# Kernel tuning notes

Hardware: AMD Instinct MI355X
Metric: run time of the kernel (lower is better)

The kernel has to match this reference:

```python
import jax, jax.numpy as jnp
import numpy as np

B, N, D = 4, 2048, 512

def setup_inputs() -> dict:
    key = jax.random.key(0)
    ks = jax.random.split(key, 7)
    s = 1.0 / np.sqrt(D)
    return {
        "x": jax.random.normal(ks[0], (B, N, D), dtype=jnp.float32),
        "Wq": jax.random.uniform(ks[1], (D, D), jnp.float32, -s, s),
        "bq": jax.random.uniform(ks[2], (D,), jnp.float32, -s, s),
        "Wk": jax.random.uniform(ks[3], (D, D), jnp.float32, -s, s),
        "bk": jax.random.uniform(ks[4], (D,), jnp.float32, -s, s),
        "Wv": jax.random.uniform(ks[5], (D, D), jnp.float32, -s, s),
        "bv": jax.random.uniform(ks[6], (D,), jnp.float32, -s, s),
    }

def reference(x, Wq, bq, Wk, bk, Wv, bv):
    # QKV projections (torch Linear: y = x @ W^T + b)
    q = jnp.einsum('bnd,ed->bne', x, Wq) + bq
    k = jnp.einsum('bnd,ed->bne', x, Wk) + bk
    v = jnp.einsum('bnd,ed->bne', x, Wv) + bv
    scale = 1.0 / jnp.sqrt(jnp.asarray(q.shape[-1], q.dtype))
    scores = jnp.einsum('bqd,bkd->bqk', q, k) * scale  # [B,N,N]
    weights = jax.nn.softmax(scores, axis=-1)
    return jnp.einsum('bqk,bkd->bqd', weights, v)
```

## Files before the change

### kernel.cpp

```cpp
#include <hip/hip_runtime.h>
#include <cstdint>
#include <cstddef>

#define SEQ 2048
#define DIM 512

using floatx4 = __attribute__((ext_vector_type(4))) float;
using halfx8  = __attribute__((ext_vector_type(8))) _Float16;

__device__ __forceinline__ ushort f2h(float f) {
    _Float16 h = (_Float16)f;
    return __builtin_bit_cast(unsigned short, h);
}

#define GLL(g, l) __builtin_amdgcn_global_load_lds( \
    (const __attribute__((address_space(1))) uint32_t*)(g), \
    (__attribute__((address_space(3))) uint32_t*)(l), 16, 0, 0)

__global__ void prep_k(const float* __restrict__ x,
                       const float* __restrict__ Wq, const float* __restrict__ Wk,
                       const float* __restrict__ Wv,
                       const float* __restrict__ bq, const float* __restrict__ bk,
                       const float* __restrict__ bv,
                       ushort* __restrict__ xh, ushort* __restrict__ wcat,
                       float* __restrict__ bcat, float* __restrict__ rowsum) {
    int i = blockIdx.x * 256 + threadIdx.x;
    if (i < 1048576) {
        float4 v = ((const float4*)x)[i];
        ((ushort4*)xh)[i] = make_ushort4(f2h(v.x), f2h(v.y), f2h(v.z), f2h(v.w));
    } else if (i < 1048576 + 196608) {
        int j = i - 1048576;
        int which = j >> 16;
        const float* w = (which == 0) ? Wq : (which == 1) ? Wk : Wv;
        float4 v = ((const float4*)w)[j & 0xFFFF];
        ((ushort4*)wcat)[j] = make_ushort4(f2h(v.x), f2h(v.y), f2h(v.z), f2h(v.w));
    } else if (i < 1048576 + 196608 + 384) {
        int j = i - 1245184;
        const float* bsrc = (j < 128) ? bq : (j < 256) ? bk : bv;
        ((float4*)bcat)[j] = ((const float4*)bsrc)[j & 127];
    } else if (i < 1048576 + 196608 + 384 + 2048) {
        int j = i - 1245568;
        ((float4*)rowsum)[j] = (float4){0.f, 0.f, 0.f, 0.f};
    }
}


template<int EPI, int TM>
__global__ __launch_bounds__(TM * 2, 4)
void gemm_k(const ushort* __restrict__ A, const ushort* __restrict__ B,
            void* __restrict__ Cout, const float* __restrict__ bias,
            float* __restrict__ rowsum, ushort* __restrict__ vt,
            int lda, int ldb, int ldc, int kIters, float alpha,
            long sA, long sB, long sC)
{
    constexpr int T = TM * 2;
    __shared__ __align__(16) ushort smem[TM * 64 + 128 * 64];
    ushort* Ps = smem;

    const int tid = threadIdx.x;
    const int bz = blockIdx.z;
    int b, kofs;
    if (EPI == 2) { b = bz & 3; kofs = (bz >> 2) * 1024; }
    else          { b = bz; kofs = 0; }
    const ushort* Ab = A + (size_t)b * sA + kofs;
    const ushort* Bb = B + (size_t)b * sB + kofs;

    const int m0 = blockIdx.y * TM;
    const int n0 = blockIdx.x * 128;
    const int lane = tid & 63, wave = tid >> 6;
    const int wm = (wave >> 1) * 64, wn = (wave & 1) * 64;
    const int quad = lane >> 4, l16 = lane & 15;
    const int swz = (l16 >> 1) & 3;

    const int sA0 = tid, sA1 = tid + T;
    const int rA0 = sA0 >> 2, rA1 = sA1 >> 2;
    const int kA0 = (sA0 & 3) ^ ((rA0 >> 1) & 3);
    const int kA1 = (sA1 & 3) ^ ((rA1 >> 1) & 3);
    const ushort* gA0 = Ab + (size_t)(m0 + rA0) * lda + kA0 * 8;
    const ushort* gA1 = Ab + (size_t)(m0 + rA1) * lda + kA1 * 8;
    const int rB0 = tid >> 2;
    const int kB0 = (tid & 3) ^ ((rB0 >> 1) & 3);
    const ushort* gB0 = Bb + (size_t)(n0 + rB0) * ldb + kB0 * 8;
    const ushort* gB1 = nullptr;
    int sB1 = 0;
    if constexpr (TM == 128) {
        sB1 = tid + 256;
        int rB1 = sB1 >> 2;
        int kB1 = (sB1 & 3) ^ ((rB1 >> 1) & 3);
        gB1 = Bb + (size_t)(n0 + rB1) * ldb + kB1 * 8;
    }

    auto STAGE = [&](int kk, int bufi) {
        int ko = kk * 32;
        ushort* Ad = smem + bufi * (TM * 32);
        ushort* Bd = smem + TM * 64 + bufi * 4096;
        GLL(gA0 + ko, Ad + sA0 * 8);
        GLL(gA1 + ko, Ad + sA1 * 8);
        GLL(gB0 + ko, Bd + tid * 8);
        if constexpr (TM == 128) GLL(gB1 + ko, Bd + sB1 * 8);
    };

    int ofsA[4], ofsB[4];
#pragma unroll
    for (int mi = 0; mi < 4; mi++)
        ofsA[mi] = ((wm + mi * 16 + l16) * 4 + (quad ^ swz)) * 8;
#pragma unroll
    for (int ni = 0; ni < 4; ni++)
        ofsB[ni] = ((wn + ni * 16 + l16) * 4 + (quad ^ swz)) * 8;

    floatx4 acc[4][4];
#pragma unroll
    for (int i = 0; i < 4; i++)
#pragma unroll
        for (int j = 0; j < 4; j++)
            acc[i][j] = (floatx4){0.f, 0.f, 0.f, 0.f};

    STAGE(0, 0);
    for (int it = 0; it < kIters; ++it) {
        __syncthreads();
        const int buf = it & 1;
        if (it + 1 < kIters) STAGE(it + 1, buf ^ 1);
        const ushort* Ad = smem + buf * (TM * 32);
        const ushort* Bd = smem + TM * 64 + buf * 4096;
        halfx8 af[4], bfr[4];
#pragma unroll
        for (int mi = 0; mi < 4; mi++) af[mi] = *(const halfx8*)&Ad[ofsA[mi]];
#pragma unroll
        for (int ni = 0; ni < 4; ni++) bfr[ni] = *(const halfx8*)&Bd[ofsB[ni]];
#pragma unroll
        for (int mi = 0; mi < 4; mi++)
#pragma unroll
            for (int ni = 0; ni < 4; ni++)
                acc[mi][ni] = __builtin_amdgcn_mfma_f32_16x16x32_f16(af[mi], bfr[ni], acc[mi][ni], 0, 0, 0);
    }

    if (EPI == 0 && n0 >= 1024) {
#pragma unroll
        for (int ni = 0; ni < 4; ni++) {
            int col = n0 + wn + ni * 16 + l16;
            float bv = bias[col];
            int e = col - 1024;
#pragma unroll
            for (int mi = 0; mi < 4; mi++) {
                int row0 = m0 + wm + mi * 16 + quad * 4;
                int bb = row0 >> 11;
                int j = row0 & 2047;
                ushort4 pk = make_ushort4(f2h(acc[mi][ni][0] + bv), f2h(acc[mi][ni][1] + bv),
                                          f2h(acc[mi][ni][2] + bv), f2h(acc[mi][ni][3] + bv));
                *(ushort4*)&vt[((size_t)(bb << 9) + e) * 2048 + j] = pk;
            }
        }
    } else {
        float bvv[4];
        if (EPI == 0) {
#pragma unroll
            for (int ni = 0; ni < 4; ni++) bvv[ni] = bias[n0 + wn + ni * 16 + l16];
        }
        float inv[4][4];
        if (EPI == 2) {
#pragma unroll
            for (int mi = 0; mi < 4; mi++)
#pragma unroll
                for (int r = 0; r < 4; r++)
                    inv[mi][r] = __builtin_amdgcn_rcpf(
                        rowsum[b * SEQ + m0 + wm + mi * 16 + quad * 4 + r]);
        }
        size_t base = (EPI == 1) ? (size_t)b * sC : (EPI == 2) ? (size_t)bz * sC : 0;
        constexpr int NPASS = TM / 128;
        __syncthreads();
#pragma unroll
        for (int p = 0; p < NPASS; ++p) {
            if (NPASS == 1 || (wm >> 7) == p) {
                int wml = wm & 127;
#pragma unroll
                for (int mi = 0; mi < 4; mi++)
#pragma unroll
                    for (int ni = 0; ni < 4; ni++) {
                        int col_l = wn + ni * 16 + l16;
                        int c = col_l >> 3, w = col_l & 7;
#pragma unroll
                        for (int r = 0; r < 4; r++) {
                            int row_l = wml + mi * 16 + quad * 4 + r;
                            float v = (EPI == 1) ? __expf(acc[mi][ni][r] * alpha)
                                    : (EPI == 2) ? acc[mi][ni][r] * inv[mi][r]
                                                 : acc[mi][ni][r] + bvv[ni];
                            Ps[row_l * 128 + ((c ^ (row_l & 7)) << 3) + w] = f2h(v);
                        }
                    }
            }
            __syncthreads();
            if constexpr (TM == 128) {
                int rr = tid >> 1, h = tid & 1;
                float s = 0.f;
                ushort* dstrow = (ushort*)Cout + base + (size_t)(m0 + rr) * ldc + n0;
#pragma unroll
                for (int j = 0; j < 8; j++) {
                    int c = h * 8 + j;
                    halfx8 pv = *(const halfx8*)&Ps[rr * 128 + ((c ^ (rr & 7)) << 3)];
                    if (EPI == 1) {
#pragma unroll
                        for (int e = 0; e < 8; e++) s += (float)pv[e];
                    }
                    *(halfx8*)(dstrow + c * 8) = pv;
                }
                if (EPI == 1) atomicAdd(&rowsum[b * SEQ + m0 + rr], s);
            } else {
                int rr = tid >> 2, t3 = tid & 3;
                float s = 0.f;
                ushort* dstrow = (ushort*)Cout + base + (size_t)(m0 + p * 128 + rr) * ldc + n0;
#pragma unroll
                for (int j = 0; j < 4; j++) {
                    int c = j * 4 + t3;
                    halfx8 pv = *(const halfx8*)&Ps[rr * 128 + ((c ^ (rr & 7)) << 3)];
                    if (EPI == 1) {
#pragma unroll
                        for (int e = 0; e < 8; e++) s += (float)pv[e];
                    }
                    *(halfx8*)(dstrow + c * 8) = pv;
                }
                if (EPI == 1) {
                    s += __shfl_xor(s, 1);
                    s += __shfl_xor(s, 2);
                    if (t3 == 0) atomicAdd(&rowsum[b * SEQ + m0 + p * 128 + rr], s);
                }
            }
            if (p + 1 < NPASS) __syncthreads();
        }
    }
}

__global__ void reduce_k(const ushort* __restrict__ part, float* __restrict__ out) {
    int t = blockIdx.x * 256 + threadIdx.x;
    size_t E = (size_t)t * 8;
    int b = (int)(E >> 20);
    size_t le = E & ((1u << 20) - 1);
    float acc[8] = {0,0,0,0,0,0,0,0};
#pragma unroll
    for (int kc = 0; kc < 2; kc++) {
        halfx8 p = *(const halfx8*)&part[(((size_t)(kc * 4 + b)) << 20) + le];
#pragma unroll
        for (int e = 0; e < 8; e++) acc[e] += (float)p[e];
    }
    float4 o0 = {acc[0], acc[1], acc[2], acc[3]};
    float4 o1 = {acc[4], acc[5], acc[6], acc[7]};
    ((float4*)(out + E))[0] = o0;
    ((float4*)(out + E))[1] = o1;
}

extern "C" void kernel_launch(void* const* d_in, const int* in_sizes, int n_in,
                              void* d_out, int out_size, void* d_ws, size_t ws_size,
                              hipStream_t stream) {
    const float* x  = (const float*)d_in[0];
    const float* Wq = (const float*)d_in[1];
    const float* bq = (const float*)d_in[2];
    const float* Wk = (const float*)d_in[3];
    const float* bk = (const float*)d_in[4];
    const float* Wv = (const float*)d_in[5];
    const float* bv = (const float*)d_in[6];
    float* out = (float*)d_out;
    char* ws = (char*)d_ws;

    ushort* partial = (ushort*)(ws);
    ushort* xh      = (ushort*)(ws);
    ushort* wcat    = (ushort*)(ws + 8388608);
    float*  bcat    = (float*)(ws + 9961472);
    float*  rowsum  = (float*)(ws + 33554432);
    ushort* Pb      = (ushort*)(ws + 33587200);
    ushort* vt      = (ushort*)(ws + 67141632);
    ushort* qkh     = (ushort*)(ws + 75530240);

    prep_k<<<4874, 256, 0, stream>>>(x, Wq, Wk, Wv, bq, bk, bv, xh, wcat, bcat, rowsum);

    gemm_k<0, 128><<<dim3(12, 64, 1), 256, 0, stream>>>(
        xh, wcat, qkh, bcat, nullptr, vt, 512, 512, 1024, 16, 1.0f, 0, 0, 0);

    const float scale = 0.04419417382415922f;
    gemm_k<1, 256><<<dim3(16, 8, 4), 512, 0, stream>>>(
        qkh, qkh + 512, Pb, nullptr, rowsum, nullptr, 1024, 1024, 2048, 16, scale,
        (long)SEQ * 1024, (long)SEQ * 1024, (long)SEQ * SEQ);

    gemm_k<2, 128><<<dim3(4, 16, 8), 256, 0, stream>>>(
        Pb, vt, partial, nullptr, rowsum, nullptr, 2048, 2048, 512, 32, 1.0f,
        (long)SEQ * SEQ, (long)DIM * SEQ, (long)SEQ * DIM);

    reduce_k<<<2048, 256, 0, stream>>>(partial, out);
}
```

Measured before the change: 167.4 us.

## Replace split-K partial buffer and reduce kernel with direct float atomics into output

The PV GEMM's split-K halves now atomically add their normalized fp32 results straight into the output, which the prep kernel zeroes beforehand. This removes the fp16 partial buffer, its round trip through memory, and the separate reduce kernel launch. It also raises the launch-bounds occupancy hints and pre-reduces row sums across lane pairs before the atomic in the TM=128 path. The cost is 4M scattered per-element float atomics plus a larger zeroing pass in prep, and a change to register pressure from the tighter occupancy bounds.

```diff
diff --git a/kernel.cpp b/kernel.cpp
--- a/kernel.cpp
+++ b/kernel.cpp
@@ -23,30 +23,34 @@
                        const float* __restrict__ bq, const float* __restrict__ bk,
                        const float* __restrict__ bv,
                        ushort* __restrict__ xh, ushort* __restrict__ wcat,
-                       float* __restrict__ bcat, float* __restrict__ rowsum) {
+                       float* __restrict__ bcat, float* __restrict__ rowsum,
+                       float* __restrict__ outz) {
     int i = blockIdx.x * 256 + threadIdx.x;
     if (i < 1048576) {
         float4 v = ((const float4*)x)[i];
         ((ushort4*)xh)[i] = make_ushort4(f2h(v.x), f2h(v.y), f2h(v.z), f2h(v.w));
-    } else if (i < 1048576 + 196608) {
+    } else if (i < 1245184) {
         int j = i - 1048576;
         int which = j >> 16;
         const float* w = (which == 0) ? Wq : (which == 1) ? Wk : Wv;
         float4 v = ((const float4*)w)[j & 0xFFFF];
         ((ushort4*)wcat)[j] = make_ushort4(f2h(v.x), f2h(v.y), f2h(v.z), f2h(v.w));
-    } else if (i < 1048576 + 196608 + 384) {
+    } else if (i < 1245568) {
         int j = i - 1245184;
         const float* bsrc = (j < 128) ? bq : (j < 256) ? bk : bv;
         ((float4*)bcat)[j] = ((const float4*)bsrc)[j & 127];
-    } else if (i < 1048576 + 196608 + 384 + 2048) {
+    } else if (i < 1247616) {
         int j = i - 1245568;
         ((float4*)rowsum)[j] = (float4){0.f, 0.f, 0.f, 0.f};
+    } else if (i < 2296192) {
+        int j = i - 1247616;
+        ((float4*)outz)[j] = (float4){0.f, 0.f, 0.f, 0.f};
     }
 }
 
 
 template<int EPI, int TM>
-__global__ __launch_bounds__(TM * 2, 4)
+__global__ __launch_bounds__(TM * 2, (TM == 128 ? 5 : 6))
 void gemm_k(const ushort* __restrict__ A, const ushort* __restrict__ B,
             void* __restrict__ Cout, const float* __restrict__ bias,
             float* __restrict__ rowsum, ushort* __restrict__ vt,
@@ -134,7 +138,27 @@
                 acc[mi][ni] = __builtin_amdgcn_mfma_f32_16x16x32_f16(af[mi], bfr[ni], acc[mi][ni], 0, 0, 0);
     }
 
-    if (EPI == 0 && n0 >= 1024) {
+    if constexpr (EPI == 2) {
+        float inv[4][4];
+#pragma unroll
+        for (int mi = 0; mi < 4; mi++)
+#pragma unroll
+            for (int r = 0; r < 4; r++)
+                inv[mi][r] = __builtin_amdgcn_rcpf(
+                    rowsum[b * SEQ + m0 + wm + mi * 16 + quad * 4 + r]);
+        float* outp = (float*)Cout + (size_t)b * sC;
+#pragma unroll
+        for (int mi = 0; mi < 4; mi++)
+#pragma unroll
+            for (int ni = 0; ni < 4; ni++) {
+                int col = n0 + wn + ni * 16 + l16;
+#pragma unroll
+                for (int r = 0; r < 4; r++) {
+                    int row = m0 + wm + mi * 16 + quad * 4 + r;
+                    atomicAdd(&outp[(size_t)row * ldc + col], acc[mi][ni][r] * inv[mi][r]);
+                }
+            }
+    } else if (EPI == 0 && n0 >= 1024) {
 #pragma unroll
         for (int ni = 0; ni < 4; ni++) {
             int col = n0 + wn + ni * 16 + l16;
@@ -156,16 +180,7 @@
 #pragma unroll
             for (int ni = 0; ni < 4; ni++) bvv[ni] = bias[n0 + wn + ni * 16 + l16];
         }
-        float inv[4][4];
-        if (EPI == 2) {
-#pragma unroll
-            for (int mi = 0; mi < 4; mi++)
-#pragma unroll
-                for (int r = 0; r < 4; r++)
-                    inv[mi][r] = __builtin_amdgcn_rcpf(
-                        rowsum[b * SEQ + m0 + wm + mi * 16 + quad * 4 + r]);
-        }
-        size_t base = (EPI == 1) ? (size_t)b * sC : (EPI == 2) ? (size_t)bz * sC : 0;
+        size_t base = (EPI == 1) ? (size_t)b * sC : 0;
         constexpr int NPASS = TM / 128;
         __syncthreads();
 #pragma unroll
@@ -182,7 +197,6 @@
                         for (int r = 0; r < 4; r++) {
                             int row_l = wml + mi * 16 + quad * 4 + r;
                             float v = (EPI == 1) ? __expf(acc[mi][ni][r] * alpha)
-                                    : (EPI == 2) ? acc[mi][ni][r] * inv[mi][r]
                                                  : acc[mi][ni][r] + bvv[ni];
                             Ps[row_l * 128 + ((c ^ (row_l & 7)) << 3) + w] = f2h(v);
                         }
@@ -203,7 +217,10 @@
                     }
                     *(halfx8*)(dstrow + c * 8) = pv;
                 }
-                if (EPI == 1) atomicAdd(&rowsum[b * SEQ + m0 + rr], s);
+                if (EPI == 1) {
+                    s += __shfl_xor(s, 1);
+                    if (h == 0) atomicAdd(&rowsum[b * SEQ + m0 + rr], s);
+                }
             } else {
                 int rr = tid >> 2, t3 = tid & 3;
                 float s = 0.f;
@@ -227,24 +244,6 @@
             if (p + 1 < NPASS) __syncthreads();
         }
     }
-}
-
-__global__ void reduce_k(const ushort* __restrict__ part, float* __restrict__ out) {
-    int t = blockIdx.x * 256 + threadIdx.x;
-    size_t E = (size_t)t * 8;
-    int b = (int)(E >> 20);
-    size_t le = E & ((1u << 20) - 1);
-    float acc[8] = {0,0,0,0,0,0,0,0};
-#pragma unroll
-    for (int kc = 0; kc < 2; kc++) {
-        halfx8 p = *(const halfx8*)&part[(((size_t)(kc * 4 + b)) << 20) + le];
-#pragma unroll
-        for (int e = 0; e < 8; e++) acc[e] += (float)p[e];
-    }
-    float4 o0 = {acc[0], acc[1], acc[2], acc[3]};
-    float4 o1 = {acc[4], acc[5], acc[6], acc[7]};
-    ((float4*)(out + E))[0] = o0;
-    ((float4*)(out + E))[1] = o1;
 }
 
 extern "C" void kernel_launch(void* const* d_in, const int* in_sizes, int n_in,
@@ -260,7 +259,6 @@
     float* out = (float*)d_out;
     char* ws = (char*)d_ws;
 
-    ushort* partial = (ushort*)(ws);
     ushort* xh      = (ushort*)(ws);
     ushort* wcat    = (ushort*)(ws + 8388608);
     float*  bcat    = (float*)(ws + 9961472);
@@ -269,7 +267,7 @@
     ushort* vt      = (ushort*)(ws + 67141632);
     ushort* qkh     = (ushort*)(ws + 75530240);
 
-    prep_k<<<4874, 256, 0, stream>>>(x, Wq, Wk, Wv, bq, bk, bv, xh, wcat, bcat, rowsum);
+    prep_k<<<8970, 256, 0, stream>>>(x, Wq, Wk, Wv, bq, bk, bv, xh, wcat, bcat, rowsum, out);
 
     gemm_k<0, 128><<<dim3(12, 64, 1), 256, 0, stream>>>(
         xh, wcat, qkh, bcat, nullptr, vt, 512, 512, 1024, 16, 1.0f, 0, 0, 0);
@@ -280,8 +278,6 @@
         (long)SEQ * 1024, (long)SEQ * 1024, (long)SEQ * SEQ);
 
     gemm_k<2, 128><<<dim3(4, 16, 8), 256, 0, stream>>>(
-        Pb, vt, partial, nullptr, rowsum, nullptr, 2048, 2048, 512, 32, 1.0f,
+        Pb, vt, out, nullptr, rowsum, nullptr, 2048, 2048, 512, 32, 1.0f,
         (long)SEQ * SEQ, (long)DIM * SEQ, (long)SEQ * DIM);
-
-    reduce_k<<<2048, 256, 0, stream>>>(partial, out);
-}
+}
```

New measurement: 318.8 us. 1.91x slower.

## Split scores GEMM into dedicated kernel with 4 waves each computing 64x128

Applied to the files above, without the earlier changes.

The QK^T scores stage moves out of the templated GEMM into its own kernel. It keeps the 256x128 block tile but uses 256 threads instead of 512, so each wave computes a 64x128 sub-tile with 32 accumulators and reuses more fragments per LDS read. The generic GEMM loses its TM template and the exp epilogue path. The larger register footprint lowers occupancy (launch bounds 2) and risks register pressure.

```diff
diff --git a/kernel.cpp b/kernel.cpp
--- a/kernel.cpp
+++ b/kernel.cpp
@@ -28,33 +28,31 @@
     if (i < 1048576) {
         float4 v = ((const float4*)x)[i];
         ((ushort4*)xh)[i] = make_ushort4(f2h(v.x), f2h(v.y), f2h(v.z), f2h(v.w));
-    } else if (i < 1048576 + 196608) {
+    } else if (i < 1245184) {
         int j = i - 1048576;
         int which = j >> 16;
         const float* w = (which == 0) ? Wq : (which == 1) ? Wk : Wv;
         float4 v = ((const float4*)w)[j & 0xFFFF];
         ((ushort4*)wcat)[j] = make_ushort4(f2h(v.x), f2h(v.y), f2h(v.z), f2h(v.w));
-    } else if (i < 1048576 + 196608 + 384) {
+    } else if (i < 1245568) {
         int j = i - 1245184;
         const float* bsrc = (j < 128) ? bq : (j < 256) ? bk : bv;
         ((float4*)bcat)[j] = ((const float4*)bsrc)[j & 127];
-    } else if (i < 1048576 + 196608 + 384 + 2048) {
+    } else if (i < 1247616) {
         int j = i - 1245568;
         ((float4*)rowsum)[j] = (float4){0.f, 0.f, 0.f, 0.f};
     }
 }
 
-
-template<int EPI, int TM>
-__global__ __launch_bounds__(TM * 2, 4)
+template<int EPI>
+__global__ __launch_bounds__(256, 4)
 void gemm_k(const ushort* __restrict__ A, const ushort* __restrict__ B,
             void* __restrict__ Cout, const float* __restrict__ bias,
             float* __restrict__ rowsum, ushort* __restrict__ vt,
-            int lda, int ldb, int ldc, int kIters, float alpha,
+            int lda, int ldb, int ldc, int kIters,
             long sA, long sB, long sC)
 {
-    constexpr int T = TM * 2;
-    __shared__ __align__(16) ushort smem[TM * 64 + 128 * 64];
+    __shared__ __align__(16) ushort smem[128 * 64 + 128 * 64];
     ushort* Ps = smem;
 
     const int tid = threadIdx.x;
@@ -65,39 +63,30 @@
     const ushort* Ab = A + (size_t)b * sA + kofs;
     const ushort* Bb = B + (size_t)b * sB + kofs;
 
-    const int m0 = blockIdx.y * TM;
+    const int m0 = blockIdx.y * 128;
     const int n0 = blockIdx.x * 128;
     const int lane = tid & 63, wave = tid >> 6;
     const int wm = (wave >> 1) * 64, wn = (wave & 1) * 64;
     const int quad = lane >> 4, l16 = lane & 15;
     const int swz = (l16 >> 1) & 3;
 
-    const int sA0 = tid, sA1 = tid + T;
+    const int sA0 = tid, sA1 = tid + 256;
     const int rA0 = sA0 >> 2, rA1 = sA1 >> 2;
     const int kA0 = (sA0 & 3) ^ ((rA0 >> 1) & 3);
     const int kA1 = (sA1 & 3) ^ ((rA1 >> 1) & 3);
     const ushort* gA0 = Ab + (size_t)(m0 + rA0) * lda + kA0 * 8;
     const ushort* gA1 = Ab + (size_t)(m0 + rA1) * lda + kA1 * 8;
-    const int rB0 = tid >> 2;
-    const int kB0 = (tid & 3) ^ ((rB0 >> 1) & 3);
-    const ushort* gB0 = Bb + (size_t)(n0 + rB0) * ldb + kB0 * 8;
-    const ushort* gB1 = nullptr;
-    int sB1 = 0;
-    if constexpr (TM == 128) {
-        sB1 = tid + 256;
-        int rB1 = sB1 >> 2;
-        int kB1 = (sB1 & 3) ^ ((rB1 >> 1) & 3);
-        gB1 = Bb + (size_t)(n0 + rB1) * ldb + kB1 * 8;
-    }
+    const ushort* gB0 = Bb + (size_t)(n0 + rA0) * ldb + kA0 * 8;
+    const ushort* gB1 = Bb + (size_t)(n0 + rA1) * ldb + kA1 * 8;
 
     auto STAGE = [&](int kk, int bufi) {
         int ko = kk * 32;
-        ushort* Ad = smem + bufi * (TM * 32);
-        ushort* Bd = smem + TM * 64 + bufi * 4096;
+        ushort* Ad = smem + bufi * 4096;
+        ushort* Bd = smem + 8192 + bufi * 4096;
         GLL(gA0 + ko, Ad + sA0 * 8);
         GLL(gA1 + ko, Ad + sA1 * 8);
-        GLL(gB0 + ko, Bd + tid * 8);
-        if constexpr (TM == 128) GLL(gB1 + ko, Bd + sB1 * 8);
+        GLL(gB0 + ko, Bd + sA0 * 8);
+        GLL(gB1 + ko, Bd + sA1 * 8);
     };
 
     int ofsA[4], ofsB[4];
@@ -120,8 +109,8 @@
         __syncthreads();
         const int buf = it & 1;
         if (it + 1 < kIters) STAGE(it + 1, buf ^ 1);
-        const ushort* Ad = smem + buf * (TM * 32);
-        const ushort* Bd = smem + TM * 64 + buf * 4096;
+        const ushort* Ad = smem + buf * 4096;
+        const ushort* Bd = smem + 8192 + buf * 4096;
         halfx8 af[4], bfr[4];
 #pragma unroll
         for (int mi = 0; mi < 4; mi++) af[mi] = *(const halfx8*)&Ad[ofsA[mi]];
@@ -165,67 +154,146 @@
                     inv[mi][r] = __builtin_amdgcn_rcpf(
                         rowsum[b * SEQ + m0 + wm + mi * 16 + quad * 4 + r]);
         }
-        size_t base = (EPI == 1) ? (size_t)b * sC : (EPI == 2) ? (size_t)bz * sC : 0;
-        constexpr int NPASS = TM / 128;
-        __syncthreads();
-#pragma unroll
-        for (int p = 0; p < NPASS; ++p) {
-            if (NPASS == 1 || (wm >> 7) == p) {
-                int wml = wm & 127;
-#pragma unroll
-                for (int mi = 0; mi < 4; mi++)
-#pragma unroll
-                    for (int ni = 0; ni < 4; ni++) {
-                        int col_l = wn + ni * 16 + l16;
-                        int c = col_l >> 3, w = col_l & 7;
-#pragma unroll
-                        for (int r = 0; r < 4; r++) {
-                            int row_l = wml + mi * 16 + quad * 4 + r;
-                            float v = (EPI == 1) ? __expf(acc[mi][ni][r] * alpha)
-                                    : (EPI == 2) ? acc[mi][ni][r] * inv[mi][r]
-                                                 : acc[mi][ni][r] + bvv[ni];
-                            Ps[row_l * 128 + ((c ^ (row_l & 7)) << 3) + w] = f2h(v);
-                        }
-                    }
-            }
-            __syncthreads();
-            if constexpr (TM == 128) {
-                int rr = tid >> 1, h = tid & 1;
-                float s = 0.f;
-                ushort* dstrow = (ushort*)Cout + base + (size_t)(m0 + rr) * ldc + n0;
-#pragma unroll
-                for (int j = 0; j < 8; j++) {
-                    int c = h * 8 + j;
-                    halfx8 pv = *(const halfx8*)&Ps[rr * 128 + ((c ^ (rr & 7)) << 3)];
-                    if (EPI == 1) {
-#pragma unroll
-                        for (int e = 0; e < 8; e++) s += (float)pv[e];
-                    }
-                    *(halfx8*)(dstrow + c * 8) = pv;
-                }
-                if (EPI == 1) atomicAdd(&rowsum[b * SEQ + m0 + rr], s);
-            } else {
-                int rr = tid >> 2, t3 = tid & 3;
-                float s = 0.f;
-                ushort* dstrow = (ushort*)Cout + base + (size_t)(m0 + p * 128 + rr) * ldc + n0;
-#pragma unroll
-                for (int j = 0; j < 4; j++) {
-                    int c = j * 4 + t3;
-                    halfx8 pv = *(const halfx8*)&Ps[rr * 128 + ((c ^ (rr & 7)) << 3)];
-                    if (EPI == 1) {
-#pragma unroll
-                        for (int e = 0; e < 8; e++) s += (float)pv[e];
-                    }
-                    *(halfx8*)(dstrow + c * 8) = pv;
-                }
-                if (EPI == 1) {
-                    s += __shfl_xor(s, 1);
-                    s += __shfl_xor(s, 2);
-                    if (t3 == 0) atomicAdd(&rowsum[b * SEQ + m0 + p * 128 + rr], s);
+        size_t base = (EPI == 2) ? (size_t)bz * sC : 0;
+        __syncthreads();
+#pragma unroll
+        for (int mi = 0; mi < 4; mi++)
+#pragma unroll
+            for (int ni = 0; ni < 4; ni++) {
+                int col_l = wn + ni * 16 + l16;
+                int c = col_l >> 3, w = col_l & 7;
+#pragma unroll
+                for (int r = 0; r < 4; r++) {
+                    int row_l = wm + mi * 16 + quad * 4 + r;
+                    float v = (EPI == 2) ? acc[mi][ni][r] * inv[mi][r]
+                                         : acc[mi][ni][r] + bvv[ni];
+                    Ps[row_l * 128 + ((c ^ (row_l & 7)) << 3) + w] = f2h(v);
                 }
             }
-            if (p + 1 < NPASS) __syncthreads();
-        }
+        __syncthreads();
+        int rr = tid >> 1, h = tid & 1;
+        ushort* dstrow = (ushort*)Cout + base + (size_t)(m0 + rr) * ldc + n0;
+#pragma unroll
+        for (int j = 0; j < 8; j++) {
+            int c = h * 8 + j;
+            halfx8 pv = *(const halfx8*)&Ps[rr * 128 + ((c ^ (rr & 7)) << 3)];
+            *(halfx8*)(dstrow + c * 8) = pv;
+        }
+    }
+}
+
+__global__ __launch_bounds__(256, 2)
+void scores_k(const ushort* __restrict__ qkh, ushort* __restrict__ P,
+              float* __restrict__ rowsum, float alpha)
+{
+    __shared__ __align__(16) ushort smem[2 * 8192 + 2 * 4096];
+    ushort* Ps = smem;
+
+    const int tid = threadIdx.x;
+    const int b = blockIdx.z;
+    const ushort* Ab = qkh + (size_t)b * (SEQ * 1024);
+    const ushort* Bb = qkh + 512 + (size_t)b * (SEQ * 1024);
+
+    const int m0 = blockIdx.y * 256;
+    const int n0 = blockIdx.x * 128;
+    const int lane = tid & 63, wave = tid >> 6;
+    const int wm = wave * 64;
+    const int quad = lane >> 4, l16 = lane & 15;
+    const int swz = (l16 >> 1) & 3;
+
+    const ushort* gA[4];
+    const ushort* gB[2];
+#pragma unroll
+    for (int j = 0; j < 4; j++) {
+        int s = tid + 256 * j, rA = s >> 2;
+        int kA = (s & 3) ^ ((rA >> 1) & 3);
+        gA[j] = Ab + (size_t)(m0 + rA) * 1024 + kA * 8;
+    }
+#pragma unroll
+    for (int j = 0; j < 2; j++) {
+        int s = tid + 256 * j, rB = s >> 2;
+        int kB = (s & 3) ^ ((rB >> 1) & 3);
+        gB[j] = Bb + (size_t)(n0 + rB) * 1024 + kB * 8;
+    }
+
+    auto STAGE = [&](int kk, int bufi) {
+        int ko = kk * 32;
+        ushort* Ad = smem + bufi * 8192;
+        ushort* Bd = smem + 16384 + bufi * 4096;
+#pragma unroll
+        for (int j = 0; j < 4; j++) GLL(gA[j] + ko, Ad + (tid + 256 * j) * 8);
+#pragma unroll
+        for (int j = 0; j < 2; j++) GLL(gB[j] + ko, Bd + (tid + 256 * j) * 8);
+    };
+
+    int ofsA[4], ofsB[8];
+#pragma unroll
+    for (int mi = 0; mi < 4; mi++)
+        ofsA[mi] = ((wm + mi * 16 + l16) * 4 + (quad ^ swz)) * 8;
+#pragma unroll
+    for (int ni = 0; ni < 8; ni++)
+        ofsB[ni] = ((ni * 16 + l16) * 4 + (quad ^ swz)) * 8;
+
+    floatx4 acc[4][8];
+#pragma unroll
+    for (int i = 0; i < 4; i++)
+#pragma unroll
+        for (int j = 0; j < 8; j++)
+            acc[i][j] = (floatx4){0.f, 0.f, 0.f, 0.f};
+
+    STAGE(0, 0);
+    for (int it = 0; it < 16; ++it) {
+        __syncthreads();
+        const int buf = it & 1;
+        if (it + 1 < 16) STAGE(it + 1, buf ^ 1);
+        const ushort* Ad = smem + buf * 8192;
+        const ushort* Bd = smem + 16384 + buf * 4096;
+        halfx8 af[4], bfr[8];
+#pragma unroll
+        for (int mi = 0; mi < 4; mi++) af[mi] = *(const halfx8*)&Ad[ofsA[mi]];
+#pragma unroll
+        for (int ni = 0; ni < 8; ni++) bfr[ni] = *(const halfx8*)&Bd[ofsB[ni]];
+#pragma unroll
+        for (int mi = 0; mi < 4; mi++)
+#pragma unroll
+            for (int ni = 0; ni < 8; ni++)
+                acc[mi][ni] = __builtin_amdgcn_mfma_f32_16x16x32_f16(af[mi], bfr[ni], acc[mi][ni], 0, 0, 0);
+    }
+
+    __syncthreads();
+#pragma unroll
+    for (int p = 0; p < 2; ++p) {
+        if ((wm >> 7) == p) {
+            int wml = wm & 127;
+#pragma unroll
+            for (int mi = 0; mi < 4; mi++)
+#pragma unroll
+                for (int ni = 0; ni < 8; ni++) {
+                    int col_l = ni * 16 + l16;
+                    int c = col_l >> 3, w = col_l & 7;
+#pragma unroll
+                    for (int r = 0; r < 4; r++) {
+                        int row_l = wml + mi * 16 + quad * 4 + r;
+                        Ps[row_l * 128 + ((c ^ (row_l & 7)) << 3) + w] =
+                            f2h(__expf(acc[mi][ni][r] * alpha));
+                    }
+                }
+        }
+        __syncthreads();
+        int rr = tid >> 1, h = tid & 1;
+        float s = 0.f;
+        ushort* dstrow = P + (size_t)b * SEQ * SEQ + (size_t)(m0 + p * 128 + rr) * 2048 + n0;
+#pragma unroll
+        for (int j = 0; j < 8; j++) {
+            int c = h * 8 + j;
+            halfx8 pv = *(const halfx8*)&Ps[rr * 128 + ((c ^ (rr & 7)) << 3)];
+#pragma unroll
+            for (int e = 0; e < 8; e++) s += (float)pv[e];
+            *(halfx8*)(dstrow + c * 8) = pv;
+        }
+        s += __shfl_xor(s, 1);
+        if (h == 0) atomicAdd(&rowsum[b * SEQ + m0 + p * 128 + rr], s);
+        if (p == 0) __syncthreads();
     }
 }
 
@@ -271,16 +339,14 @@
 
     prep_k<<<4874, 256, 0, stream>>>(x, Wq, Wk, Wv, bq, bk, bv, xh, wcat, bcat, rowsum);
 
-    gemm_k<0, 128><<<dim3(12, 64, 1), 256, 0, stream>>>(
-        xh, wcat, qkh, bcat, nullptr, vt, 512, 512, 1024, 16, 1.0f, 0, 0, 0);
+    gemm_k<0><<<dim3(12, 64, 1), 256, 0, stream>>>(
+        xh, wcat, qkh, bcat, nullptr, vt, 512, 512, 1024, 16, 0, 0, 0);
 
     const float scale = 0.04419417382415922f;
-    gemm_k<1, 256><<<dim3(16, 8, 4), 512, 0, stream>>>(
-        qkh, qkh + 512, Pb, nullptr, rowsum, nullptr, 1024, 1024, 2048, 16, scale,
-        (long)SEQ * 1024, (long)SEQ * 1024, (long)SEQ * SEQ);
-
-    gemm_k<2, 128><<<dim3(4, 16, 8), 256, 0, stream>>>(
-        Pb, vt, partial, nullptr, rowsum, nullptr, 2048, 2048, 512, 32, 1.0f,
+    scores_k<<<dim3(16, 8, 4), 256, 0, stream>>>(qkh, Pb, rowsum, scale);
+
+    gemm_k<2><<<dim3(4, 16, 8), 256, 0, stream>>>(
+        Pb, vt, partial, nullptr, rowsum, nullptr, 2048, 2048, 512, 32,
         (long)SEQ * SEQ, (long)DIM * SEQ, (long)SEQ * DIM);
 
     reduce_k<<<2048, 256, 0, stream>>>(partial, out);
```

Result: slower. 173.8 us (+3.8%).
